# Optimization experiments

Hardware: AMD Instinct MI355X
Metric: run time of the kernel (lower is better)

The kernel has to match this reference:

```python
import jax, jax.numpy as jnp
import numpy as np
import math

B, N, D = 2, 2048, 1024
H = 16
HD = D // H
WINDOW = 256
LN_EPS = 1e-5
NEG_INF = float('-inf')


def _alibi_slopes(num_heads):
    # num_heads=16 is a power of two -> no extra-slope branch
    closest = 2 ** math.floor(math.log2(num_heads))
    base = 2.0 ** (-(2.0 ** (-(math.log2(closest) - 3))))
    return np.power(base, np.arange(1, closest + 1, dtype=np.float32))


def setup_inputs() -> dict:
    key = jax.random.key(0)
    ks = jax.random.split(key, 8)
    s = 0.02
    return {
        'x': jax.random.normal(ks[0], (B, N, D), dtype=jnp.float32),
        'qkv_w': jax.random.normal(ks[1], (D, 3 * D), dtype=jnp.float32) * s,
        'qkv_b': jnp.zeros((3 * D,), jnp.float32),
        'proj_w': jax.random.normal(ks[2], (D, D), dtype=jnp.float32) * s,
        'proj_b': jnp.zeros((D,), jnp.float32),
        'ln1_g': jnp.ones((D,), jnp.float32),
        'ln1_b': jnp.zeros((D,), jnp.float32),
        'ln2_g': jnp.ones((D,), jnp.float32),
        'ln2_b': jnp.zeros((D,), jnp.float32),
        'fc1_w': jax.random.normal(ks[3], (D, 4 * D), dtype=jnp.float32) * s,
        'fc1_b': jnp.zeros((4 * D,), jnp.float32),
        'fc2_w': jax.random.normal(ks[4], (4 * D, D), dtype=jnp.float32) * s,
        'fc2_b': jnp.zeros((D,), jnp.float32),
    }


def _layernorm(x, g, b):
    mu = jnp.mean(x, axis=-1, keepdims=True)
    var = jnp.mean(jnp.square(x - mu), axis=-1, keepdims=True)
    return (x - mu) * jax.lax.rsqrt(var + LN_EPS) * g + b


def reference(x, qkv_w, qkv_b, proj_w, proj_b, ln1_g, ln1_b, ln2_g, ln2_b,
              fc1_w, fc1_b, fc2_w, fc2_b):
    # ---- ALiBi sliding-window causal attention (pre-norm) ----
    h = _layernorm(x, ln1_g, ln1_b)
    qkv = (h @ qkv_w + qkv_b).reshape(B, N, 3, H, HD)
    q, k, v = [jnp.transpose(qkv[:, :, i], (0, 2, 1, 3)) for i in range(3)]  # [B,H,N,HD]

    scale = HD ** -0.5
    attn = jnp.einsum('bhqd,bhkd->bhqk', q, k) * scale  # [B,H,N,N]

    pos = jnp.arange(N)
    rel = pos[None, :] - pos[:, None]                      # rel[i,j] = j - i
    slopes = jnp.asarray(_alibi_slopes(H))                 # [H]
    a = slopes[:, None, None] * jnp.abs(rel).astype(jnp.float32)
    alibi = jnp.where(rel < 0, -a, a)                      # == slopes * rel
    attn = attn + alibi[None]

    # sliding-window mask: +1.0 inside window (faithful to ones-init), -inf outside
    sw = jnp.where(jnp.abs(rel) >= WINDOW, NEG_INF, 1.0)
    attn = attn + sw[None, None]

    # causal mask
    attn = jnp.where((rel > 0)[None, None], NEG_INF, attn)

    p = jax.nn.softmax(attn, axis=-1)
    o = jnp.einsum('bhqk,bhkd->bhqd', p, v)
    o = jnp.transpose(o, (0, 2, 1, 3)).reshape(B, N, D)
    x = x + (o @ proj_w + proj_b)

    # ---- FFN (Linear -> exact GELU -> Linear), pre-norm residual ----
    h2 = _layernorm(x, ln2_g, ln2_b)
    ff = jax.nn.gelu(h2 @ fc1_w + fc1_b, approximate=False) @ fc2_w + fc2_b
    return x + ff
```

## Files before the change

kernel.cpp:

```cpp
#include <hip/hip_runtime.h>
#include <stdint.h>

typedef unsigned short u16;
typedef __attribute__((ext_vector_type(8))) short bf16x8;
typedef __attribute__((ext_vector_type(4))) float f32x4;

__device__ __forceinline__ u16 f2bf(float f) {
  union { float f; unsigned u; } x; x.f = f;
  unsigned r = x.u + 0x7fffu + ((x.u >> 16) & 1u);
  return (u16)(r >> 16);
}

#define GLOAD16(g, l) __builtin_amdgcn_global_load_lds( \
    (const __attribute__((address_space(1))) unsigned int*)(g), \
    (__attribute__((address_space(3))) unsigned int*)(l), 16, 0, 0)

__global__ __launch_bounds__(256) void wt_kernel(const float* __restrict__ W,
                                                 u16* __restrict__ Wt, int K, int N) {
  __shared__ float tile[32][33];
  int tx = threadIdx.x & 31, ty = threadIdx.x >> 5;
  int n0 = blockIdx.x * 32, k0 = blockIdx.y * 32;
#pragma unroll
  for (int i = 0; i < 32; i += 8)
    tile[ty + i][tx] = W[(size_t)(k0 + ty + i) * N + n0 + tx];
  __syncthreads();
#pragma unroll
  for (int i = 0; i < 32; i += 8)
    Wt[(size_t)(n0 + ty + i) * K + k0 + tx] = f2bf(tile[tx][ty + i]);
}

__global__ __launch_bounds__(256) void ln_kernel(const float* __restrict__ x,
                                                 const float* __restrict__ g,
                                                 const float* __restrict__ be,
                                                 u16* __restrict__ out) {
  int row = blockIdx.x, t = threadIdx.x;
  const float4 v = ((const float4*)(x + (size_t)row * 1024))[t];
  float s = v.x + v.y + v.z + v.w;
#pragma unroll
  for (int m = 1; m < 64; m <<= 1) s += __shfl_xor(s, m);
  __shared__ float p1[4], p2[4];
  int wid = t >> 6, lane = t & 63;
  if (lane == 0) p1[wid] = s;
  __syncthreads();
  float mean = (p1[0] + p1[1] + p1[2] + p1[3]) * (1.f / 1024.f);
  float a0 = v.x - mean, a1 = v.y - mean, a2 = v.z - mean, a3 = v.w - mean;
  float ss = a0 * a0 + a1 * a1 + a2 * a2 + a3 * a3;
#pragma unroll
  for (int m = 1; m < 64; m <<= 1) ss += __shfl_xor(ss, m);
  if (lane == 0) p2[wid] = ss;
  __syncthreads();
  float var = (p2[0] + p2[1] + p2[2] + p2[3]) * (1.f / 1024.f);
  float rs = rsqrtf(var + 1e-5f);
  const float4 gg = ((const float4*)g)[t];
  const float4 bb = ((const float4*)be)[t];
  ushort4 ov;
  ov.x = f2bf(a0 * rs * gg.x + bb.x);
  ov.y = f2bf(a1 * rs * gg.y + bb.y);
  ov.z = f2bf(a2 * rs * gg.z + bb.z);
  ov.w = f2bf(a3 * rs * gg.w + bb.w);
  *(ushort4*)(out + (size_t)row * 1024 + t * 4) = ov;
}

template <int BN, int GELU_F, int HAS_RES, int OUT_F32, int OUT_BF16>
__global__ __launch_bounds__(256) void gemm_kernel(
    const u16* __restrict__ A, const u16* __restrict__ Bt,
    const float* __restrict__ bias, const float* __restrict__ res,
    float* __restrict__ outf, u16* __restrict__ outb, int M, int N, int K) {
  __shared__ u16 lA[2][128 * 64];
  __shared__ u16 lB[2][BN * 64];
  const int t = threadIdx.x, lane = t & 63, wid = t >> 6;
  const int bm = blockIdx.x, bn = blockIdx.y;
  constexpr int FM = (BN == 128) ? 4 : 2;
  const int wr = (BN == 128) ? (wid >> 1) : wid;
  const int wc = (BN == 128) ? (wid & 1) : 0;
  f32x4 acc[FM][4] = {};

  const int nkt = K >> 6;

  auto stage = [&](int buf, int kt) {
#pragma unroll
    for (int r = 0; r < 4; ++r) {
      int f = (r * 256 + t) * 16;
      int fs = f ^ (((f >> 7) & 7) << 4);
      int row = fs >> 7;
      int kb = (fs & 127) >> 1;
      GLOAD16(A + (size_t)(bm * 128 + row) * K + kt * 64 + kb,
              ((char*)&lA[buf][0]) + (r * 256 + wid * 64) * 16);
    }
#pragma unroll
    for (int r = 0; r < BN / 32; ++r) {
      int f = (r * 256 + t) * 16;
      int fs = f ^ (((f >> 7) & 7) << 4);
      int row = fs >> 7;
      int kb = (fs & 127) >> 1;
      GLOAD16(Bt + (size_t)(bn * BN + row) * K + kt * 64 + kb,
              ((char*)&lB[buf][0]) + (r * 256 + wid * 64) * 16);
    }
  };

  stage(0, 0);
  __syncthreads();

  for (int kt = 0; kt < nkt; ++kt) {
    const int cur = kt & 1;
    if (kt + 1 < nkt) stage(cur ^ 1, kt + 1);
#pragma unroll
    for (int kk = 0; kk < 2; ++kk) {
      bf16x8 af[FM], bfr[4];
#pragma unroll
      for (int fm = 0; fm < FM; ++fm) {
        int row = wr * (FM * 16) + fm * 16 + (lane & 15);
        int k = kk * 32 + (lane >> 4) * 8;
        af[fm] = *(const bf16x8*)((const char*)&lA[cur][0] + ((row * 128 + k * 2) ^ ((row & 7) << 4)));
      }
#pragma unroll
      for (int fn = 0; fn < 4; ++fn) {
        int row = wc * 64 + fn * 16 + (lane & 15);
        int k = kk * 32 + (lane >> 4) * 8;
        bfr[fn] = *(const bf16x8*)((const char*)&lB[cur][0] + ((row * 128 + k * 2) ^ ((row & 7) << 4)));
      }
#pragma unroll
      for (int fm = 0; fm < FM; ++fm)
#pragma unroll
        for (int fn = 0; fn < 4; ++fn)
          acc[fm][fn] = __builtin_amdgcn_mfma_f32_16x16x32_bf16(af[fm], bfr[fn], acc[fm][fn], 0, 0, 0);
    }
    __syncthreads();
  }

#pragma unroll
  for (int fm = 0; fm < FM; ++fm) {
#pragma unroll
    for (int fn = 0; fn < 4; ++fn) {
      int col = bn * BN + wc * 64 + fn * 16 + (lane & 15);
      float bcol = bias[col];
#pragma unroll
      for (int r = 0; r < 4; ++r) {
        int row = bm * 128 + wr * (FM * 16) + fm * 16 + (lane >> 4) * 4 + r;
        float v = acc[fm][fn][r] + bcol;
        if constexpr (GELU_F) v = 0.5f * v * (1.0f + erff(v * 0.70710678118654752f));
        size_t idx = (size_t)row * N + col;
        if constexpr (HAS_RES) v += res[idx];
        if constexpr (OUT_F32) outf[idx] = v;
        if constexpr (OUT_BF16) outb[idx] = f2bf(v);
      }
    }
  }
}

__global__ __launch_bounds__(256) void attn_kernel(const u16* __restrict__ qkv,
                                                   u16* __restrict__ o) {
  __shared__ u16 kvbuf[22016];
  __shared__ u16 lP[4][16 * 296];
  u16* lK = kvbuf;
  u16* lV = kvbuf;
  const int t = threadIdx.x, lane = t & 63, w = t >> 6;
  const int qtile = blockIdx.x, bh = blockIdx.y, b = bh >> 4, h = bh & 15;
  const int kbase = qtile * 64 - 256;
  const size_t bq = (size_t)b * 2048 * 3072;
  const float NEGBIG = -1e30f;

  for (int r = 0; r < 10; ++r) {
    int jl = r * 32 + (t >> 3);
    int d0 = (t & 7) * 8;
    int jg = kbase + jl;
    uint4 kv;
    if (jg >= 0 && jg < 2048)
      kv = *(const uint4*)(qkv + bq + (size_t)jg * 3072 + 1024 + h * 64 + d0);
    else
      kv = make_uint4(0, 0, 0, 0);
    *(uint4*)((char*)lK + ((jl * 128 + d0 * 2) ^ ((jl & 7) << 4))) = kv;
  }
  __syncthreads();

  const int i0 = qtile * 64 + w * 16;
  const int q15 = lane & 15, grp = lane >> 4;
  const u16* qrow = qkv + bq + (size_t)(i0 + q15) * 3072 + h * 64;
  bf16x8 qf0 = *(const bf16x8*)(qrow + grp * 8);
  bf16x8 qf1 = *(const bf16x8*)(qrow + 32 + grp * 8);

  f32x4 st[17];
#pragma unroll
  for (int tt = 0; tt < 17; ++tt) {
    st[tt] = f32x4{0.f, 0.f, 0.f, 0.f};
    int klb = w * 16 + tt * 16;
#pragma unroll
    for (int kk = 0; kk < 2; ++kk) {
      int row = klb + q15;
      int k = kk * 32 + grp * 8;
      bf16x8 kf = *(const bf16x8*)((const char*)lK + ((row * 128 + k * 2) ^ ((row & 7) << 4)));
      st[tt] = __builtin_amdgcn_mfma_f32_16x16x32_bf16(kf, (kk ? qf1 : qf0), st[tt], 0, 0, 0);
    }
  }

  const float slope = exp2f(-0.5f * (float)(h + 1));
  const int qg = i0 + q15;
  float mx = NEGBIG;
#pragma unroll
  for (int tt = 0; tt < 17; ++tt) {
    int kb = kbase + w * 16 + tt * 16;
#pragma unroll
    for (int r = 0; r < 4; ++r) {
      int key = kb + grp * 4 + r;
      float s = st[tt][r] * 0.125f + slope * (float)(key - qg);
      bool valid = (key >= 0) && (key <= qg) && (qg - key < 256);
      s = valid ? s : NEGBIG;
      st[tt][r] = s;
      mx = fmaxf(mx, s);
    }
  }
  mx = fmaxf(mx, __shfl_xor(mx, 16));
  mx = fmaxf(mx, __shfl_xor(mx, 32));
  float sum = 0.f;
#pragma unroll
  for (int tt = 0; tt < 17; ++tt)
#pragma unroll
    for (int r = 0; r < 4; ++r) {
      float p = __expf(st[tt][r] - mx);
      st[tt][r] = p;
      sum += p;
    }
  sum += __shfl_xor(sum, 16);
  sum += __shfl_xor(sum, 32);
  const float inv = 1.0f / sum;

  u16* Pw = &lP[w][0];
#pragma unroll
  for (int tt = 0; tt < 17; ++tt) {
    unsigned u0 = ((unsigned)f2bf(st[tt][1]) << 16) | f2bf(st[tt][0]);
    unsigned u1 = ((unsigned)f2bf(st[tt][3]) << 16) | f2bf(st[tt][2]);
    uint2 uu; uu.x = u0; uu.y = u1;
    *(uint2*)(Pw + q15 * 296 + tt * 16 + grp * 4) = uu;
  }
  { uint2 z; z.x = 0; z.y = 0; *(uint2*)(Pw + q15 * 296 + 272 + grp * 4) = z; }

  __syncthreads();

  for (int r = 0; r < 11; ++r) {
    int jl = r * 32 + (t >> 3);
    int d0 = (t & 7) * 8;
    int jg = kbase + jl;
    if (jl < 336) {
      uint4 vv;
      if (jg >= 0 && jg < 2048)
        vv = *(const uint4*)(qkv + bq + (size_t)jg * 3072 + 2048 + h * 64 + d0);
      else
        vv = make_uint4(0, 0, 0, 0);
      const u16* vs = (const u16*)&vv;
#pragma unroll
      for (int u = 0; u < 8; ++u) lV[(d0 + u) * 344 + jl] = vs[u];
    }
  }
  __syncthreads();

  f32x4 ot[4] = {};
#pragma unroll
  for (int c = 0; c < 9; ++c) {
    bf16x8 pf = *(const bf16x8*)(Pw + q15 * 296 + c * 32 + grp * 8);
#pragma unroll
    for (int hb = 0; hb < 4; ++hb) {
      bf16x8 vf = *(const bf16x8*)(lV + (hb * 16 + q15) * 344 + w * 16 + c * 32 + grp * 8);
      ot[hb] = __builtin_amdgcn_mfma_f32_16x16x32_bf16(vf, pf, ot[hb], 0, 0, 0);
    }
  }

#pragma unroll
  for (int hb = 0; hb < 4; ++hb) {
    ushort4 ov;
    ov.x = f2bf(ot[hb][0] * inv);
    ov.y = f2bf(ot[hb][1] * inv);
    ov.z = f2bf(ot[hb][2] * inv);
    ov.w = f2bf(ot[hb][3] * inv);
    *(ushort4*)(o + (size_t)(b * 2048 + i0 + q15) * 1024 + h * 64 + hb * 16 + grp * 4) = ov;
  }
}

extern "C" void kernel_launch(void* const* d_in, const int* in_sizes, int n_in,
                              void* d_out, int out_size, void* d_ws, size_t ws_size,
                              hipStream_t stream) {
  const float* x      = (const float*)d_in[0];
  const float* qkv_w  = (const float*)d_in[1];
  const float* qkv_b  = (const float*)d_in[2];
  const float* proj_w = (const float*)d_in[3];
  const float* proj_b = (const float*)d_in[4];
  const float* ln1_g  = (const float*)d_in[5];
  const float* ln1_b  = (const float*)d_in[6];
  const float* ln2_g  = (const float*)d_in[7];
  const float* ln2_b  = (const float*)d_in[8];
  const float* fc1_w  = (const float*)d_in[9];
  const float* fc1_b  = (const float*)d_in[10];
  const float* fc2_w  = (const float*)d_in[11];
  const float* fc2_b  = (const float*)d_in[12];
  float* out = (float*)d_out;

  char* ws = (char*)d_ws;
  u16* qkvw_t  = (u16*)(ws);
  u16* projw_t = (u16*)(ws + 6291456);
  u16* fc1w_t  = (u16*)(ws + 8388608);
  u16* fc2w_t  = (u16*)(ws + 16777216);
  char* BIG    = ws + 25165824;
  char* SMALL  = ws + 58720256;
  u16* qkvb = (u16*)BIG;
  u16* ff1  = (u16*)BIG;
  u16* h1   = (u16*)SMALL;
  u16* obuf = (u16*)SMALL;
  u16* h2   = (u16*)SMALL;
  float* x1 = out;

  wt_kernel<<<dim3(96, 32), 256, 0, stream>>>(qkv_w, qkvw_t, 1024, 3072);
  wt_kernel<<<dim3(32, 32), 256, 0, stream>>>(proj_w, projw_t, 1024, 1024);
  wt_kernel<<<dim3(128, 32), 256, 0, stream>>>(fc1_w, fc1w_t, 1024, 4096);
  wt_kernel<<<dim3(32, 128), 256, 0, stream>>>(fc2_w, fc2w_t, 4096, 1024);

  ln_kernel<<<4096, 256, 0, stream>>>(x, ln1_g, ln1_b, h1);
  gemm_kernel<128, 0, 0, 0, 1><<<dim3(32, 24), 256, 0, stream>>>(h1, qkvw_t, qkv_b, nullptr, nullptr, qkvb, 4096, 3072, 1024);
  attn_kernel<<<dim3(32, 32), 256, 0, stream>>>(qkvb, obuf);
  gemm_kernel<64, 0, 1, 1, 0><<<dim3(32, 16), 256, 0, stream>>>(obuf, projw_t, proj_b, x, x1, nullptr, 4096, 1024, 1024);
  ln_kernel<<<4096, 256, 0, stream>>>(x1, ln2_g, ln2_b, h2);
  gemm_kernel<128, 1, 0, 0, 1><<<dim3(32, 32), 256, 0, stream>>>(h2, fc1w_t, fc1_b, nullptr, nullptr, ff1, 4096, 4096, 1024);
  gemm_kernel<64, 0, 1, 1, 0><<<dim3(32, 16), 256, 0, stream>>>(ff1, fc2w_t, fc2_b, x1, out, nullptr, 4096, 1024, 4096);
}
```

Measured before the change: 332.1 us.

## Fuse preprocessing kernels, add XCD-swizzled GEMM, fast GELU, retune small-N GEMM tiles

Merges the weight transpose launches and the first layernorm into one kernel, cutting launch overhead. Adds a single-buffered 128x128 GEMM with XCD-aware block remapping for the QKV and FC1 projections to improve L2 locality. Replaces exact erf GELU with a tanh approximation and uses 32-wide N tiles for proj and FC2 GEMMs to increase block count. The tanh GELU changes numerics, and single buffering removes load/compute overlap in the new GEMM.

```diff
diff --git a/kernel.cpp b/kernel.cpp
--- a/kernel.cpp
+++ b/kernel.cpp
@@ -11,22 +11,70 @@
   return (u16)(r >> 16);
 }
 
+__device__ __forceinline__ float gelu_fast(float v) {
+  float y = 0.7978845608f * (v + 0.044715f * v * v * v);
+  float e = __expf(2.0f * y);
+  float th = 1.0f - 2.0f / (e + 1.0f);
+  return 0.5f * v * (1.0f + th);
+}
+
 #define GLOAD16(g, l) __builtin_amdgcn_global_load_lds( \
     (const __attribute__((address_space(1))) unsigned int*)(g), \
     (__attribute__((address_space(3))) unsigned int*)(l), 16, 0, 0)
 
-__global__ __launch_bounds__(256) void wt_kernel(const float* __restrict__ W,
-                                                 u16* __restrict__ Wt, int K, int N) {
+__global__ __launch_bounds__(256) void pre_kernel(
+    const float* __restrict__ qkv_w, const float* __restrict__ proj_w,
+    const float* __restrict__ fc1_w, const float* __restrict__ fc2_w,
+    u16* __restrict__ qkvw_t, u16* __restrict__ projw_t,
+    u16* __restrict__ fc1w_t, u16* __restrict__ fc2w_t,
+    const float* __restrict__ x, const float* __restrict__ g,
+    const float* __restrict__ be, u16* __restrict__ h1) {
   __shared__ float tile[32][33];
-  int tx = threadIdx.x & 31, ty = threadIdx.x >> 5;
-  int n0 = blockIdx.x * 32, k0 = blockIdx.y * 32;
-#pragma unroll
-  for (int i = 0; i < 32; i += 8)
-    tile[ty + i][tx] = W[(size_t)(k0 + ty + i) * N + n0 + tx];
-  __syncthreads();
-#pragma unroll
-  for (int i = 0; i < 32; i += 8)
-    Wt[(size_t)(n0 + ty + i) * K + k0 + tx] = f2bf(tile[tx][ty + i]);
+  __shared__ float p1[4], p2[4];
+  const int bid = blockIdx.x, t = threadIdx.x;
+  if (bid < 12288) {
+    const float* W; u16* Wt; int K, N, base, nb;
+    if (bid < 3072)      { W = qkv_w;  Wt = qkvw_t;  K = 1024; N = 3072; base = 0;    nb = 96; }
+    else if (bid < 4096) { W = proj_w; Wt = projw_t; K = 1024; N = 1024; base = 3072; nb = 32; }
+    else if (bid < 8192) { W = fc1_w;  Wt = fc1w_t;  K = 1024; N = 4096; base = 4096; nb = 128; }
+    else                 { W = fc2_w;  Wt = fc2w_t;  K = 4096; N = 1024; base = 8192; nb = 32; }
+    int r = bid - base;
+    int n0 = (r % nb) * 32, k0 = (r / nb) * 32;
+    int tx = t & 31, ty = t >> 5;
+#pragma unroll
+    for (int i = 0; i < 32; i += 8)
+      tile[ty + i][tx] = W[(size_t)(k0 + ty + i) * N + n0 + tx];
+    __syncthreads();
+#pragma unroll
+    for (int i = 0; i < 32; i += 8)
+      Wt[(size_t)(n0 + ty + i) * K + k0 + tx] = f2bf(tile[tx][ty + i]);
+  } else {
+    int row = bid - 12288;
+    const float4 v = ((const float4*)(x + (size_t)row * 1024))[t];
+    float s = v.x + v.y + v.z + v.w;
+#pragma unroll
+    for (int m = 1; m < 64; m <<= 1) s += __shfl_xor(s, m);
+    int wid = t >> 6, lane = t & 63;
+    if (lane == 0) p1[wid] = s;
+    __syncthreads();
+    float mean = (p1[0] + p1[1] + p1[2] + p1[3]) * (1.f / 1024.f);
+    float a0 = v.x - mean, a1 = v.y - mean, a2 = v.z - mean, a3 = v.w - mean;
+    float ss = a0 * a0 + a1 * a1 + a2 * a2 + a3 * a3;
+#pragma unroll
+    for (int m = 1; m < 64; m <<= 1) ss += __shfl_xor(ss, m);
+    if (lane == 0) p2[wid] = ss;
+    __syncthreads();
+    float var = (p2[0] + p2[1] + p2[2] + p2[3]) * (1.f / 1024.f);
+    float rs = rsqrtf(var + 1e-5f);
+    const float4 gg = ((const float4*)g)[t];
+    const float4 bb = ((const float4*)be)[t];
+    ushort4 ov;
+    ov.x = f2bf(a0 * rs * gg.x + bb.x);
+    ov.y = f2bf(a1 * rs * gg.y + bb.y);
+    ov.z = f2bf(a2 * rs * gg.z + bb.z);
+    ov.w = f2bf(a3 * rs * gg.w + bb.w);
+    *(ushort4*)(h1 + (size_t)row * 1024 + t * 4) = ov;
+  }
 }
 
 __global__ __launch_bounds__(256) void ln_kernel(const float* __restrict__ x,
@@ -61,6 +109,78 @@
   *(ushort4*)(out + (size_t)row * 1024 + t * 4) = ov;
 }
 
+template <int GELU_F, int HAS_RES, int OUT_F32, int OUT_BF16>
+__global__ __launch_bounds__(256) void gemm97_kernel(
+    const u16* __restrict__ A, const u16* __restrict__ Bt,
+    const float* __restrict__ bias, const float* __restrict__ res,
+    float* __restrict__ outf, u16* __restrict__ outb, int M, int N, int K, int nbn) {
+  __shared__ u16 lA[128 * 64];
+  __shared__ u16 lB[128 * 64];
+  const int t = threadIdx.x, lane = t & 63, wid = t >> 6;
+  const int wr = wid >> 1, wc = wid & 1;
+  const int nwg = gridDim.x;
+  const int q = nwg >> 3, rm = nwg & 7;
+  const int xcd = blockIdx.x & 7, oin = blockIdx.x >> 3;
+  const int swz = (xcd < rm ? xcd * (q + 1) : rm * (q + 1) + (xcd - rm) * q) + oin;
+  const int bm = swz / nbn, bn = swz % nbn;
+  f32x4 acc[4][4] = {};
+  const int nkt = K >> 6;
+
+  for (int kt = 0; kt < nkt; ++kt) {
+#pragma unroll
+    for (int r = 0; r < 4; ++r) {
+      int f = (r * 256 + t) * 16;
+      int fs = f ^ (((f >> 7) & 7) << 4);
+      int row = fs >> 7;
+      int kb = (fs & 127) >> 1;
+      GLOAD16(A + (size_t)(bm * 128 + row) * K + kt * 64 + kb, ((char*)lA) + f);
+      GLOAD16(Bt + (size_t)(bn * 128 + row) * K + kt * 64 + kb, ((char*)lB) + f);
+    }
+    __syncthreads();
+#pragma unroll
+    for (int kk = 0; kk < 2; ++kk) {
+      bf16x8 af[4], bfr[4];
+#pragma unroll
+      for (int fm = 0; fm < 4; ++fm) {
+        int row = wr * 64 + fm * 16 + (lane & 15);
+        int k = kk * 32 + (lane >> 4) * 8;
+        af[fm] = *(const bf16x8*)((const char*)lA + ((row * 128 + k * 2) ^ ((row & 7) << 4)));
+      }
+#pragma unroll
+      for (int fn = 0; fn < 4; ++fn) {
+        int row = wc * 64 + fn * 16 + (lane & 15);
+        int k = kk * 32 + (lane >> 4) * 8;
+        bfr[fn] = *(const bf16x8*)((const char*)lB + ((row * 128 + k * 2) ^ ((row & 7) << 4)));
+      }
+#pragma unroll
+      for (int fm = 0; fm < 4; ++fm)
+#pragma unroll
+        for (int fn = 0; fn < 4; ++fn)
+          acc[fm][fn] = __builtin_amdgcn_mfma_f32_16x16x32_bf16(af[fm], bfr[fn], acc[fm][fn], 0, 0, 0);
+    }
+    __syncthreads();
+  }
+
+#pragma unroll
+  for (int fm = 0; fm < 4; ++fm) {
+#pragma unroll
+    for (int fn = 0; fn < 4; ++fn) {
+      int col = bn * 128 + wc * 64 + fn * 16 + (lane & 15);
+      float bcol = bias[col];
+#pragma unroll
+      for (int r = 0; r < 4; ++r) {
+        int row = bm * 128 + wr * 64 + fm * 16 + (lane >> 4) * 4 + r;
+        float v = acc[fm][fn][r] + bcol;
+        if constexpr (GELU_F) v = gelu_fast(v);
+        size_t idx = (size_t)row * N + col;
+        if constexpr (HAS_RES) v += res[idx];
+        if constexpr (OUT_F32) outf[idx] = v;
+        if constexpr (OUT_BF16) outb[idx] = f2bf(v);
+      }
+    }
+  }
+}
+
 template <int BN, int GELU_F, int HAS_RES, int OUT_F32, int OUT_BF16>
 __global__ __launch_bounds__(256) void gemm_kernel(
     const u16* __restrict__ A, const u16* __restrict__ Bt,
@@ -71,9 +191,10 @@
   const int t = threadIdx.x, lane = t & 63, wid = t >> 6;
   const int bm = blockIdx.x, bn = blockIdx.y;
   constexpr int FM = (BN == 128) ? 4 : 2;
+  constexpr int FN = (BN == 128) ? 4 : (BN / 16);
   const int wr = (BN == 128) ? (wid >> 1) : wid;
   const int wc = (BN == 128) ? (wid & 1) : 0;
-  f32x4 acc[FM][4] = {};
+  f32x4 acc[FM][FN] = {};
 
   const int nkt = K >> 6;
 
@@ -85,7 +206,7 @@
       int row = fs >> 7;
       int kb = (fs & 127) >> 1;
       GLOAD16(A + (size_t)(bm * 128 + row) * K + kt * 64 + kb,
-              ((char*)&lA[buf][0]) + (r * 256 + wid * 64) * 16);
+              ((char*)&lA[buf][0]) + f);
     }
 #pragma unroll
     for (int r = 0; r < BN / 32; ++r) {
@@ -94,7 +215,7 @@
       int row = fs >> 7;
       int kb = (fs & 127) >> 1;
       GLOAD16(Bt + (size_t)(bn * BN + row) * K + kt * 64 + kb,
-              ((char*)&lB[buf][0]) + (r * 256 + wid * 64) * 16);
+              ((char*)&lB[buf][0]) + f);
     }
   };
 
@@ -106,7 +227,7 @@
     if (kt + 1 < nkt) stage(cur ^ 1, kt + 1);
 #pragma unroll
     for (int kk = 0; kk < 2; ++kk) {
-      bf16x8 af[FM], bfr[4];
+      bf16x8 af[FM], bfr[FN];
 #pragma unroll
       for (int fm = 0; fm < FM; ++fm) {
         int row = wr * (FM * 16) + fm * 16 + (lane & 15);
@@ -114,7 +235,7 @@
         af[fm] = *(const bf16x8*)((const char*)&lA[cur][0] + ((row * 128 + k * 2) ^ ((row & 7) << 4)));
       }
 #pragma unroll
-      for (int fn = 0; fn < 4; ++fn) {
+      for (int fn = 0; fn < FN; ++fn) {
         int row = wc * 64 + fn * 16 + (lane & 15);
         int k = kk * 32 + (lane >> 4) * 8;
         bfr[fn] = *(const bf16x8*)((const char*)&lB[cur][0] + ((row * 128 + k * 2) ^ ((row & 7) << 4)));
@@ -122,7 +243,7 @@
 #pragma unroll
       for (int fm = 0; fm < FM; ++fm)
 #pragma unroll
-        for (int fn = 0; fn < 4; ++fn)
+        for (int fn = 0; fn < FN; ++fn)
           acc[fm][fn] = __builtin_amdgcn_mfma_f32_16x16x32_bf16(af[fm], bfr[fn], acc[fm][fn], 0, 0, 0);
     }
     __syncthreads();
@@ -131,14 +252,14 @@
 #pragma unroll
   for (int fm = 0; fm < FM; ++fm) {
 #pragma unroll
-    for (int fn = 0; fn < 4; ++fn) {
+    for (int fn = 0; fn < FN; ++fn) {
       int col = bn * BN + wc * 64 + fn * 16 + (lane & 15);
       float bcol = bias[col];
 #pragma unroll
       for (int r = 0; r < 4; ++r) {
         int row = bm * 128 + wr * (FM * 16) + fm * 16 + (lane >> 4) * 4 + r;
         float v = acc[fm][fn][r] + bcol;
-        if constexpr (GELU_F) v = 0.5f * v * (1.0f + erff(v * 0.70710678118654752f));
+        if constexpr (GELU_F) v = gelu_fast(v);
         size_t idx = (size_t)row * N + col;
         if constexpr (HAS_RES) v += res[idx];
         if constexpr (OUT_F32) outf[idx] = v;
@@ -307,16 +428,13 @@
   u16* h2   = (u16*)SMALL;
   float* x1 = out;
 
-  wt_kernel<<<dim3(96, 32), 256, 0, stream>>>(qkv_w, qkvw_t, 1024, 3072);
-  wt_kernel<<<dim3(32, 32), 256, 0, stream>>>(proj_w, projw_t, 1024, 1024);
-  wt_kernel<<<dim3(128, 32), 256, 0, stream>>>(fc1_w, fc1w_t, 1024, 4096);
-  wt_kernel<<<dim3(32, 128), 256, 0, stream>>>(fc2_w, fc2w_t, 4096, 1024);
-
-  ln_kernel<<<4096, 256, 0, stream>>>(x, ln1_g, ln1_b, h1);
-  gemm_kernel<128, 0, 0, 0, 1><<<dim3(32, 24), 256, 0, stream>>>(h1, qkvw_t, qkv_b, nullptr, nullptr, qkvb, 4096, 3072, 1024);
+  pre_kernel<<<16384, 256, 0, stream>>>(qkv_w, proj_w, fc1_w, fc2_w,
+                                        qkvw_t, projw_t, fc1w_t, fc2w_t,
+                                        x, ln1_g, ln1_b, h1);
+  gemm97_kernel<0, 0, 0, 1><<<768, 256, 0, stream>>>(h1, qkvw_t, qkv_b, nullptr, nullptr, qkvb, 4096, 3072, 1024, 24);
   attn_kernel<<<dim3(32, 32), 256, 0, stream>>>(qkvb, obuf);
-  gemm_kernel<64, 0, 1, 1, 0><<<dim3(32, 16), 256, 0, stream>>>(obuf, projw_t, proj_b, x, x1, nullptr, 4096, 1024, 1024);
+  gemm_kernel<32, 0, 1, 1, 0><<<dim3(32, 32), 256, 0, stream>>>(obuf, projw_t, proj_b, x, x1, nullptr, 4096, 1024, 1024);
   ln_kernel<<<4096, 256, 0, stream>>>(x1, ln2_g, ln2_b, h2);
-  gemm_kernel<128, 1, 0, 0, 1><<<dim3(32, 32), 256, 0, stream>>>(h2, fc1w_t, fc1_b, nullptr, nullptr, ff1, 4096, 4096, 1024);
-  gemm_kernel<64, 0, 1, 1, 0><<<dim3(32, 16), 256, 0, stream>>>(ff1, fc2w_t, fc2_b, x1, out, nullptr, 4096, 1024, 4096);
-}
+  gemm97_kernel<1, 0, 0, 1><<<1024, 256, 0, stream>>>(h2, fc1w_t, fc1_b, nullptr, nullptr, ff1, 4096, 4096, 1024, 32);
+  gemm_kernel<32, 0, 1, 1, 0><<<dim3(32, 32), 256, 0, stream>>>(ff1, fc2w_t, fc2_b, x1, out, nullptr, 4096, 1024, 4096);
+}
```

Result: slower. 339.3 us (+2.2%).
